# Performance work log

Measured on AMD Instinct MI355X. Metric: run time of the kernel, lower is better.

## Reference

```python
import jax, jax.numpy as jnp
import numpy as np

D_MODEL = 1024
NUM_HEADS = 16
D_K = D_MODEL // NUM_HEADS
SCALE = float(np.sqrt(D_K))


def setup_inputs() -> dict:
    key = jax.random.key(0)
    ks = jax.random.split(key, 11)
    B, S = 2, 2048
    s = 0.02
    return {
        "query": jax.random.normal(ks[0], (B, S, D_MODEL), dtype=jnp.float32),
        "key_in": jax.random.normal(ks[1], (B, S, D_MODEL), dtype=jnp.float32),
        "value": jax.random.normal(ks[2], (B, S, D_MODEL), dtype=jnp.float32),
        "w_q": jax.random.normal(ks[3], (D_MODEL, D_MODEL), dtype=jnp.float32) * s,
        "b_q": jnp.zeros((D_MODEL,), dtype=jnp.float32),
        "w_k": jax.random.normal(ks[4], (D_MODEL, D_MODEL), dtype=jnp.float32) * s,
        "b_k": jnp.zeros((D_MODEL,), dtype=jnp.float32),
        "w_v": jax.random.normal(ks[5], (D_MODEL, D_MODEL), dtype=jnp.float32) * s,
        "b_v": jnp.zeros((D_MODEL,), dtype=jnp.float32),
        "w_o": jax.random.normal(ks[6], (D_MODEL, D_MODEL), dtype=jnp.float32) * s,
        "b_o": jnp.zeros((D_MODEL,), dtype=jnp.float32),
    }


def _mha(query, key_in, value, w_q, b_q, w_k, b_k, w_v, b_v, w_o, b_o):
    B, S, _ = query.shape
    # linear projections (x @ W + b), split into heads: [B, H, S, Dk]
    def proj(x, w, b):
        y = x @ w + b
        return y.reshape(B, -1, NUM_HEADS, D_K).transpose(0, 2, 1, 3)

    Q = proj(query, w_q, b_q)
    K = proj(key_in, w_k, b_k)
    V = proj(value, w_v, b_v)

    # scores: [B, H, Sq, Sk]
    scores = jnp.einsum("bhqd,bhkd->bhqk", Q, K) / SCALE
    attn = jax.nn.softmax(scores, axis=-1)  # dropout is identity in eval mode
    out = jnp.einsum("bhqk,bhkd->bhqd", attn, V)
    out = out.transpose(0, 2, 1, 3).reshape(B, S, D_MODEL)
    return out @ w_o + b_o


def reference(query, key_in, value, w_q, b_q, w_k, b_k, w_v, b_v, w_o, b_o):
    return _mha(query, key_in, value, w_q, b_q, w_k, b_k, w_v, b_v, w_o, b_o)
```

## Files before the change

kernel.cpp:

```cpp
#include <hip/hip_runtime.h>
#include <cstdint>

#define S_LEN 2048
#define DMODEL 1024
#define NHEADS 16
#define DK 64
#define BATCH 2
#define M_TOT 4096
#define NSPLIT 2
#define BHS (BATCH * NHEADS * S_LEN)

typedef __attribute__((ext_vector_type(8)))  short  short8;
typedef __attribute__((ext_vector_type(4)))  float  f32x4;
typedef __attribute__((ext_vector_type(16))) float  f32x16;

__device__ __forceinline__ ushort f2bf(float f) {
    union { float f; uint32_t u; } v; v.f = f;
    uint32_t r = (v.u + 0x7fffu + ((v.u >> 16) & 1u)) >> 16;
    return (ushort)r;
}
__device__ __forceinline__ float bf2f(ushort u) {
    union { uint32_t u; float f; } v; v.u = ((uint32_t)u) << 16;
    return v.f;
}
__device__ __forceinline__ float max3f(float a, float b, float c) {
    float d;
    asm("v_max3_f32 %0, %1, %2, %3" : "=v"(d) : "v"(a), "v"(b), "v"(c));
    return d;
}

__device__ __forceinline__ void gl_lds16(const void* g, void* l) {
    __builtin_amdgcn_global_load_lds(
        (const __attribute__((address_space(1))) void*)(g),
        (__attribute__((address_space(3))) void*)(l), 16, 0, 0);
}

__global__ __launch_bounds__(256)
void conv3_kernel(const float* __restrict__ a0, const float* __restrict__ a1,
                  const float* __restrict__ a2, ushort* __restrict__ o0,
                  ushort* __restrict__ o1, ushort* __restrict__ o2, int n8)
{
    const float*  in  = blockIdx.z == 0 ? a0 : (blockIdx.z == 1 ? a1 : a2);
    ushort*       out = blockIdx.z == 0 ? o0 : (blockIdx.z == 1 ? o1 : o2);
    int i = blockIdx.x * 256 + threadIdx.x;
    const int stride = gridDim.x * 256;
    for (; i < n8; i += stride) {
        const float4* p = (const float4*)(in + (size_t)i * 8);
        float4 a = p[0], b = p[1];
        ushort r[8];
        r[0]=f2bf(a.x); r[1]=f2bf(a.y); r[2]=f2bf(a.z); r[3]=f2bf(a.w);
        r[4]=f2bf(b.x); r[5]=f2bf(b.y); r[6]=f2bf(b.z); r[7]=f2bf(b.w);
        *(ushort4*)(out + (size_t)i * 8)     = *(ushort4*)&r[0];
        *(ushort4*)(out + (size_t)i * 8 + 4) = *(ushort4*)&r[4];
    }
}

__global__ __launch_bounds__(256)
void wtrans4_kernel(const float* __restrict__ wq, const float* __restrict__ wk,
                    const float* __restrict__ wv, const float* __restrict__ wo,
                    ushort* __restrict__ oq, ushort* __restrict__ ok,
                    ushort* __restrict__ ov, ushort* __restrict__ oo_hi,
                    ushort* __restrict__ oo_lo)
{
    const int z = blockIdx.z;
    const float* w  = z == 0 ? wq : (z == 1 ? wk : (z == 2 ? wv : wo));
    ushort*      hi = z == 0 ? oq : (z == 1 ? ok : (z == 2 ? ov : oo_hi));
    const bool   LO = (z == 3);

    __shared__ float t[64][65];
    const int n0 = blockIdx.x * 64, k0 = blockIdx.y * 64;
    const int r  = threadIdx.x >> 2;
    const int cb = (threadIdx.x & 3) * 16;

    #pragma unroll
    for (int j = 0; j < 4; ++j) {
        float4 v = *(const float4*)(w + (size_t)(k0 + r) * DMODEL + n0 + cb + j * 4);
        t[r][cb + j*4 + 0] = v.x;
        t[r][cb + j*4 + 1] = v.y;
        t[r][cb + j*4 + 2] = v.z;
        t[r][cb + j*4 + 3] = v.w;
    }
    __syncthreads();

    ushort h8[16], l8[16];
    #pragma unroll
    for (int j = 0; j < 16; ++j) {
        float x = t[cb + j][r];
        ushort h = f2bf(x);
        h8[j] = h;
        l8[j] = f2bf(x - bf2f(h));
    }
    ushort* dsth = hi + (size_t)(n0 + r) * DMODEL + k0 + cb;
    #pragma unroll
    for (int j = 0; j < 4; ++j)
        *(ushort4*)(dsth + j*4) = *(ushort4*)&h8[j*4];
    if (LO) {
        ushort* dstl = oo_lo + (size_t)(n0 + r) * DMODEL + k0 + cb;
        #pragma unroll
        for (int j = 0; j < 4; ++j)
            *(ushort4*)(dstl + j*4) = *(ushort4*)&l8[j*4];
    }
}

__global__ __launch_bounds__(256)
void gemm_qkv_kernel(const ushort* __restrict__ Aq, const ushort* __restrict__ Ak,
                     const ushort* __restrict__ Av, const ushort* __restrict__ Wq,
                     const ushort* __restrict__ Wk, const ushort* __restrict__ Wv,
                     const float* __restrict__ bq, const float* __restrict__ bk,
                     const float* __restrict__ bv, ushort* __restrict__ Qh,
                     ushort* __restrict__ Kh, ushort* __restrict__ Vt, float qscale)
{
    const int z = blockIdx.z;
    const ushort* A    = z == 0 ? Aq : (z == 1 ? Ak : Av);
    const ushort* Bt   = z == 0 ? Wq : (z == 1 ? Wk : Wv);
    const float*  bias = z == 0 ? bq : (z == 1 ? bk : bv);
    ushort*       out  = z == 0 ? Qh : (z == 1 ? Kh : Vt);
    const float oscale = z == 0 ? qscale : 1.0f;
    const int   mode   = z == 2 ? 2 : 1;

    __shared__ __align__(16) ushort lds[2][12288];

    const int t = threadIdx.x, wv = t >> 6, lane = t & 63;
    const int c = lane & 15, g = lane >> 4;
    const int m0 = blockIdx.y * 128, n0 = blockIdx.x * 64;
    const int wr = wv >> 1, wc = wv & 1;
    const int lrow = lane >> 3, lcol = lane & 7;

    f32x4 acc[4][2];
    #pragma unroll
    for (int i = 0; i < 4; ++i)
        #pragma unroll
        for (int j = 0; j < 2; ++j)
            acc[i][j] = (f32x4){0.f, 0.f, 0.f, 0.f};

    auto stage = [&](int buf, int kt) {
        #pragma unroll
        for (int j = 0; j < 6; ++j) {
            const int ci = wv * 6 + j;
            ushort* dst = &lds[buf][ci * 512];
            const ushort* src;
            if (ci < 16) {
                const int row  = ci * 8 + lrow;
                const int colb = (lcol * 16) ^ ((row & 7) << 4);
                src = A + (size_t)(m0 + row) * 1024 + kt * 64 + (colb >> 1);
            } else {
                const int row  = (ci - 16) * 8 + lrow;
                const int colb = (lcol * 16) ^ ((row & 7) << 4);
                src = Bt + (size_t)(n0 + row) * 1024 + kt * 64 + (colb >> 1);
            }
            gl_lds16(src, dst);
        }
    };

    stage(0, 0);
    __syncthreads();

    for (int kt = 0; kt < 16; ++kt) {
        const int cur = kt & 1;
        if (kt < 15) stage(cur ^ 1, kt + 1);

        const char* la = (const char*)&lds[cur][0];
        const char* lb = (const char*)&lds[cur][8192];
        #pragma unroll
        for (int kk = 0; kk < 2; ++kk) {
            short8 af[4], bf[2];
            #pragma unroll
            for (int mf = 0; mf < 4; ++mf) {
                const int row = wr * 64 + mf * 16 + c;
                af[mf] = *(const short8*)(la + row * 128 +
                          ((kk * 64 + g * 16) ^ ((c & 7) << 4)));
            }
            #pragma unroll
            for (int nf = 0; nf < 2; ++nf) {
                const int row = wc * 32 + nf * 16 + c;
                bf[nf] = *(const short8*)(lb + row * 128 +
                          ((kk * 64 + g * 16) ^ ((c & 7) << 4)));
            }
            #pragma unroll
            for (int mf = 0; mf < 4; ++mf)
                #pragma unroll
                for (int nf = 0; nf < 2; ++nf)
                    acc[mf][nf] = __builtin_amdgcn_mfma_f32_16x16x32_bf16(
                        af[mf], bf[nf], acc[mf][nf], 0, 0, 0);
        }
        __syncthreads();
    }

    const int b      = m0 >> 11;
    const int s_base = m0 & 2047;
    #pragma unroll
    for (int nf = 0; nf < 2; ++nf) {
        const int ncol = n0 + wc * 32 + nf * 16 + c;
        const float bv = bias[ncol];
        const int h = ncol >> 6, dk = ncol & 63;
        #pragma unroll
        for (int mf = 0; mf < 4; ++mf) {
            if (mode == 1) {
                #pragma unroll
                for (int j = 0; j < 4; ++j) {
                    const int s = s_base + wr * 64 + mf * 16 + g * 4 + j;
                    out[(((size_t)(b * NHEADS + h) * S_LEN + s) * DK) + dk] =
                        f2bf((acc[mf][nf][j] + bv) * oscale);
                }
            } else {
                ushort4 v4;
                v4.x = f2bf(acc[mf][nf][0] + bv);
                v4.y = f2bf(acc[mf][nf][1] + bv);
                v4.z = f2bf(acc[mf][nf][2] + bv);
                v4.w = f2bf(acc[mf][nf][3] + bv);
                const int s = s_base + wr * 64 + mf * 16 + g * 4;
                *(ushort4*)&out[((size_t)(b * NHEADS + h) * DK + dk) * S_LEN + s] = v4;
            }
        }
    }
}

__global__ __launch_bounds__(256)
void gemm_o2_kernel(const ushort* __restrict__ A, const ushort* __restrict__ Bhi,
                    const ushort* __restrict__ Blo, const float* __restrict__ bias,
                    float* __restrict__ out)
{
    __shared__ __align__(16) ushort lds[2][16384];

    const int t = threadIdx.x, wv = t >> 6, lane = t & 63;
    const int c = lane & 15, g = lane >> 4;
    const int m0 = blockIdx.y * 128, n0 = blockIdx.x * 64;
    const int wr = wv >> 1, wc = wv & 1;
    const int lrow = lane >> 3, lcol = lane & 7;

    f32x4 acc[4][2];
    #pragma unroll
    for (int i = 0; i < 4; ++i)
        #pragma unroll
        for (int j = 0; j < 2; ++j)
            acc[i][j] = (f32x4){0.f, 0.f, 0.f, 0.f};

    auto stage = [&](int buf, int kt) {
        #pragma unroll
        for (int j = 0; j < 8; ++j) {
            const int ci = wv * 8 + j;
            ushort* dst = &lds[buf][ci * 512];
            const ushort* src;
            if (ci < 16) {
                const int row  = ci * 8 + lrow;
                const int colb = (lcol * 16) ^ ((row & 7) << 4);
                src = A + (size_t)(m0 + row) * 1024 + kt * 64 + (colb >> 1);
            } else if (ci < 24) {
                const int row  = (ci - 16) * 8 + lrow;
                const int colb = (lcol * 16) ^ ((row & 7) << 4);
                src = Bhi + (size_t)(n0 + row) * 1024 + kt * 64 + (colb >> 1);
            } else {
                const int row  = (ci - 24) * 8 + lrow;
                const int colb = (lcol * 16) ^ ((row & 7) << 4);
                src = Blo + (size_t)(n0 + row) * 1024 + kt * 64 + (colb >> 1);
            }
            gl_lds16(src, dst);
        }
    };

    stage(0, 0);
    __syncthreads();

    for (int kt = 0; kt < 16; ++kt) {
        const int cur = kt & 1;
        if (kt < 15) stage(cur ^ 1, kt + 1);

        const char* la = (const char*)&lds[cur][0];
        const char* lh = (const char*)&lds[cur][8192];
        const char* ll = (const char*)&lds[cur][12288];
        #pragma unroll
        for (int kk = 0; kk < 2; ++kk) {
            short8 af[4], bh[2], bl[2];
            #pragma unroll
            for (int mf = 0; mf < 4; ++mf) {
                const int row = wr * 64 + mf * 16 + c;
                af[mf] = *(const short8*)(la + row * 128 +
                          ((kk * 64 + g * 16) ^ ((c & 7) << 4)));
            }
            #pragma unroll
            for (int nf = 0; nf < 2; ++nf) {
                const int row = wc * 32 + nf * 16 + c;
                const int off = row * 128 + ((kk * 64 + g * 16) ^ ((c & 7) << 4));
                bh[nf] = *(const short8*)(lh + off);
                bl[nf] = *(const short8*)(ll + off);
            }
            #pragma unroll
            for (int mf = 0; mf < 4; ++mf)
                #pragma unroll
                for (int nf = 0; nf < 2; ++nf) {
                    acc[mf][nf] = __builtin_amdgcn_mfma_f32_16x16x32_bf16(af[mf], bh[nf], acc[mf][nf], 0,0,0);
                    acc[mf][nf] = __builtin_amdgcn_mfma_f32_16x16x32_bf16(af[mf], bl[nf], acc[mf][nf], 0,0,0);
                }
        }
        __syncthreads();
    }

    #pragma unroll
    for (int nf = 0; nf < 2; ++nf) {
        const int ncol = n0 + wc * 32 + nf * 16 + c;
        const float bv = bias[ncol];
        #pragma unroll
        for (int mf = 0; mf < 4; ++mf)
            #pragma unroll
            for (int j = 0; j < 4; ++j) {
                const int m = m0 + wr * 64 + mf * 16 + g * 4 + j;
                out[(size_t)m * 1024 + ncol] = acc[mf][nf][j] + bv;
            }
    }
}

__global__ __launch_bounds__(256, 2)
void attn_split_kernel(const ushort* __restrict__ Qh, const ushort* __restrict__ Kh,
                       const ushort* __restrict__ Vt, ushort* __restrict__ Op,
                       float* __restrict__ msave, float* __restrict__ lsave)
{
    __shared__ __align__(16) ushort KV[2][8192];

    const int t  = threadIdx.x, wv = t >> 6, lane = t & 63;
    const int q  = lane & 31;
    const int hi = lane >> 5;
    const int bh = blockIdx.y;
    const int q0 = blockIdx.x * 128 + wv * 32;
    const int split = blockIdx.z;
    const int kbase = split * (S_LEN / NSPLIT);

    const ushort* Kb = Kh + (size_t)bh * S_LEN * DK;
    const ushort* Vb = Vt + (size_t)bh * DK * S_LEN;
    const ushort* Qb = Qh + ((size_t)bh * S_LEN + q0 + q) * DK;

    short8 qf[4];
    #pragma unroll
    for (int s = 0; s < 4; ++s)
        qf[s] = *(const short8*)(Qb + s * 16 + hi * 8);

    const ushort* sbase[4];
    int sstr[4];
    char* dbase[4];
    #pragma unroll
    for (int j = 0; j < 4; ++j) {
        const int D = (j * 256 + t) * 16;
        dbase[j] = (char*)&KV[0][0] + D;
        if (D < 8192) {
            const int row = D >> 7;
            const int X   = D & 127;
            const int Xs  = X ^ ((((row & 7) ^ ((row >> 3) & 3))) << 4);
            sbase[j] = Kb + row * DK + (Xs >> 1);
            sstr[j]  = DK;
        } else {
            const int Y   = D - 8192;
            const int kk  = Y >> 12;
            const int Z   = Y & 4095;
            const int r   = Z >> 7;
            const int gsl = ((Z & 127) >> 4) ^ ((r & 7) ^ ((r >> 3) & 3));
            const int d   = r + ((gsl >> 2) << 5);
            sbase[j] = Vb + (size_t)d * S_LEN + kk * 32 + (gsl & 3) * 8;
            sstr[j]  = 1;
        }
    }
    auto stage = [&](int buf, int k0) {
        #pragma unroll
        for (int j = 0; j < 4; ++j)
            gl_lds16(sbase[j] + (size_t)k0 * sstr[j], dbase[j] + buf * 16384);
    };

    float m = -3.0e38f, l = 0.f;
    f32x16 accO[2];
    #pragma unroll
    for (int i = 0; i < 16; ++i) { accO[0][i] = 0.f; accO[1][i] = 0.f; }

    const int swz = ((q & 7) ^ ((q >> 3) & 3)) << 4;

    stage(0, kbase);
    __syncthreads();

    const int NT = S_LEN / NSPLIT / 64;
    for (int kt = 0; kt < NT; ++kt) {
        const int cur = kt & 1;
        if (kt < NT - 1) stage(cur ^ 1, kbase + (kt + 1) * 64);

        const char* Kl = (const char*)&KV[cur][0];
        const char* Vl = Kl + 8192;

        #pragma unroll
        for (int kk = 0; kk < 2; ++kk) {
            f32x16 sa;
            #pragma unroll
            for (int i = 0; i < 16; ++i) sa[i] = 0.f;
            #pragma unroll
            for (int s = 0; s < 4; ++s) {
                short8 kf = *(const short8*)(Kl + (kk * 32 + q) * 128 +
                                             ((s * 32 + hi * 16) ^ swz));
                sa = __builtin_amdgcn_mfma_f32_32x32x16_bf16(kf, qf[s], sa, 0, 0, 0);
            }

            float m0_ = max3f(sa[0],  sa[1],  sa[2]);
            float m1_ = max3f(sa[3],  sa[4],  sa[5]);
            float m2_ = max3f(sa[6],  sa[7],  sa[8]);
            float m3_ = max3f(sa[9],  sa[10], sa[11]);
            float m4_ = max3f(sa[12], sa[13], sa[14]);
            float mt  = fmaxf(max3f(m0_, m1_, m2_), max3f(m3_, m4_, sa[15]));
            mt = fmaxf(mt, __shfl_xor(mt, 32));

            if (__any(mt > m + 8.f)) {
                const float mnew = fmaxf(m, mt);
                const float corr = __builtin_amdgcn_exp2f(m - mnew);
                #pragma unroll
                for (int r = 0; r < 16; ++r) { accO[0][r] *= corr; accO[1][r] *= corr; }
                l *= corr;
                m = mnew;
            }

            float p[16], ps = 0.f;
            #pragma unroll
            for (int r = 0; r < 16; ++r) {
                p[r] = __builtin_amdgcn_exp2f(sa[r] - m);
                ps += p[r];
            }
            ps += __shfl_xor(ps, 32);
            l += ps;

            uint32_t u[8];
            #pragma unroll
            for (int jj = 0; jj < 8; ++jj)
                asm("v_cvt_pk_bf16_f32 %0, %1, %2"
                    : "=v"(u[jj]) : "v"(p[2*jj]), "v"(p[2*jj+1]));
            asm("v_permlane32_swap_b32 %0, %1" : "+v"(u[0]), "+v"(u[2]));
            asm("v_permlane32_swap_b32 %0, %1" : "+v"(u[1]), "+v"(u[3]));
            asm("v_permlane32_swap_b32 %0, %1" : "+v"(u[4]), "+v"(u[6]));
            asm("v_permlane32_swap_b32 %0, %1" : "+v"(u[5]), "+v"(u[7]));
            union { uint32_t w[4]; short8 s8; } pb0, pb1;
            pb0.w[0]=u[0]; pb0.w[1]=u[1]; pb0.w[2]=u[2]; pb0.w[3]=u[3];
            pb1.w[0]=u[4]; pb1.w[1]=u[5]; pb1.w[2]=u[6]; pb1.w[3]=u[7];

            const char* Vg = Vl + kk * 4096;
            #pragma unroll
            for (int db = 0; db < 2; ++db) {
                short8 vf0 = *(const short8*)(Vg + q * 128 + ((db*64 +      hi*16) ^ swz));
                short8 vf1 = *(const short8*)(Vg + q * 128 + ((db*64 + 32 + hi*16) ^ swz));
                accO[db] = __builtin_amdgcn_mfma_f32_32x32x16_bf16(vf0, pb0.s8, accO[db], 0, 0, 0);
                accO[db] = __builtin_amdgcn_mfma_f32_32x32x16_bf16(vf1, pb1.s8, accO[db], 0, 0, 0);
            }
        }
        __syncthreads();
    }

    const float inv = 1.f / l;
    const size_t sIdx = ((size_t)split * BATCH * NHEADS + bh) * S_LEN + q0 + q;
    ushort* base = Op + sIdx * DK;
    #pragma unroll
    for (int db = 0; db < 2; ++db)
        #pragma unroll
        for (int r = 0; r < 16; ++r) {
            const int d = db * 32 + (r & 3) + 8 * (r >> 2) + 4 * hi;
            base[d] = f2bf(accO[db][r] * inv);
        }
    if (hi == 0) {
        msave[sIdx] = m;
        lsave[sIdx] = l;
    }
}

__global__ __launch_bounds__(256)
void combine_kernel(const ushort* __restrict__ Op, const float* __restrict__ msave,
                    const float* __restrict__ lsave, ushort* __restrict__ ctx)
{
    const int idx = blockIdx.x * 256 + threadIdx.x;
    const int bh = idx >> 11;
    const int s  = idx & 2047;

    const float m1 = msave[idx],        l1 = lsave[idx];
    const float m2 = msave[BHS + idx],  l2 = lsave[BHS + idx];
    const float mmax = fmaxf(m1, m2);
    const float w1 = l1 * __builtin_amdgcn_exp2f(m1 - mmax);
    const float w2 = l2 * __builtin_amdgcn_exp2f(m2 - mmax);
    const float inv = 1.f / (w1 + w2);
    const float r1 = w1 * inv, r2 = w2 * inv;

    const ushort* o1 = Op + (size_t)idx * DK;
    const ushort* o2 = Op + ((size_t)BHS + idx) * DK;
    const int b = bh >> 4, h = bh & 15;
    ushort* dst = ctx + ((size_t)b * S_LEN + s) * DMODEL + h * DK;

    #pragma unroll
    for (int j = 0; j < 8; ++j) {
        ushort4 a = *(const ushort4*)(o1 + j * 8);
        ushort4 bq = *(const ushort4*)(o1 + j * 8 + 4);
        ushort4 c = *(const ushort4*)(o2 + j * 8);
        ushort4 dq = *(const ushort4*)(o2 + j * 8 + 4);
        ushort r[8];
        r[0] = f2bf(r1 * bf2f(a.x) + r2 * bf2f(c.x));
        r[1] = f2bf(r1 * bf2f(a.y) + r2 * bf2f(c.y));
        r[2] = f2bf(r1 * bf2f(a.z) + r2 * bf2f(c.z));
        r[3] = f2bf(r1 * bf2f(a.w) + r2 * bf2f(c.w));
        r[4] = f2bf(r1 * bf2f(bq.x) + r2 * bf2f(dq.x));
        r[5] = f2bf(r1 * bf2f(bq.y) + r2 * bf2f(dq.y));
        r[6] = f2bf(r1 * bf2f(bq.z) + r2 * bf2f(dq.z));
        r[7] = f2bf(r1 * bf2f(bq.w) + r2 * bf2f(dq.w));
        *(ushort4*)(dst + j * 8)     = *(ushort4*)&r[0];
        *(ushort4*)(dst + j * 8 + 4) = *(ushort4*)&r[4];
    }
}

extern "C" void kernel_launch(void* const* d_in, const int* in_sizes, int n_in,
                              void* d_out, int out_size, void* d_ws, size_t ws_size,
                              hipStream_t stream)
{
    const float* query  = (const float*)d_in[0];
    const float* key_in = (const float*)d_in[1];
    const float* value  = (const float*)d_in[2];
    const float* w_q = (const float*)d_in[3];
    const float* b_q = (const float*)d_in[4];
    const float* w_k = (const float*)d_in[5];
    const float* b_k = (const float*)d_in[6];
    const float* w_v = (const float*)d_in[7];
    const float* b_v = (const float*)d_in[8];
    const float* w_o = (const float*)d_in[9];
    const float* b_o = (const float*)d_in[10];
    float* out = (float*)d_out;

    const size_t E4M = (size_t)M_TOT * DMODEL;
    const size_t E1M = (size_t)DMODEL * DMODEL;

    ushort* ws = (ushort*)d_ws;
    ushort* Aq    = ws;
    ushort* Ak    = Aq + E4M;
    ushort* Av    = Ak + E4M;
    ushort* Qh    = Av + E4M;
    ushort* Kh    = Qh + E4M;
    ushort* Vt    = Kh + E4M;
    ushort* Wq    = Vt + E4M;
    ushort* Wk    = Wq + E1M;
    ushort* Wv    = Wk + E1M;
    ushort* Wo_hi = Wv + E1M;
    ushort* Wo_lo = Wo_hi + E1M;
    float*  msave = (float*)(Wo_lo + E1M);
    float*  lsave = msave + (size_t)NSPLIT * BHS;
    ushort* ctx   = Aq;
    ushort* Op    = Ak;

    const float qscale = 0.125f * 1.44269504088896340736f;

    dim3 blk(256);
    hipLaunchKernelGGL(conv3_kernel, dim3(512, 1, 3), blk, 0, stream,
                       query, key_in, value, Aq, Ak, Av, (int)(E4M / 8));
    hipLaunchKernelGGL(wtrans4_kernel, dim3(16, 16, 4), blk, 0, stream,
                       w_q, w_k, w_v, w_o, Wq, Wk, Wv, Wo_hi, Wo_lo);

    dim3 ggrd(DMODEL / 64, M_TOT / 128, 3);
    hipLaunchKernelGGL(gemm_qkv_kernel, ggrd, blk, 0, stream,
                       Aq, Ak, Av, Wq, Wk, Wv, b_q, b_k, b_v, Qh, Kh, Vt, qscale);

    dim3 agrd(S_LEN / 128, BATCH * NHEADS, NSPLIT);
    hipLaunchKernelGGL(attn_split_kernel, agrd, blk, 0, stream,
                       Qh, Kh, Vt, Op, msave, lsave);

    hipLaunchKernelGGL(combine_kernel, dim3(BHS / 256), blk, 0, stream,
                       Op, msave, lsave, ctx);

    dim3 ogrd(DMODEL / 64, M_TOT / 128);
    hipLaunchKernelGGL(gemm_o2_kernel, ogrd, blk, 0, stream,
                       ctx, Wo_hi, Wo_lo, b_o, out);
}
```

Measured before the change: 138.2 us.

## Drop split-bf16 output weight and double attention block size to 512 threads

The output projection no longer splits W_o into high and low bf16 halves. It uses a single bf16 weight, which halves its MFMA count and its weight staging and drops the low-part transpose writes. Separately, the attention kernel now runs 512-thread blocks that each cover 256 queries, so every K/V tile staged in LDS is shared by twice as many waves. The cost is lower precision in the output GEMM and different occupancy for attention, since launch_bounds changes from (256,2) to (512).

Result: faster. 133.9 us (-3.2%).

```diff
diff --git a/kernel.cpp b/kernel.cpp
--- a/kernel.cpp
+++ b/kernel.cpp
@@ -59,13 +59,11 @@
 void wtrans4_kernel(const float* __restrict__ wq, const float* __restrict__ wk,
                     const float* __restrict__ wv, const float* __restrict__ wo,
                     ushort* __restrict__ oq, ushort* __restrict__ ok,
-                    ushort* __restrict__ ov, ushort* __restrict__ oo_hi,
-                    ushort* __restrict__ oo_lo)
+                    ushort* __restrict__ ov, ushort* __restrict__ oo)
 {
     const int z = blockIdx.z;
     const float* w  = z == 0 ? wq : (z == 1 ? wk : (z == 2 ? wv : wo));
-    ushort*      hi = z == 0 ? oq : (z == 1 ? ok : (z == 2 ? ov : oo_hi));
-    const bool   LO = (z == 3);
+    ushort*      hi = z == 0 ? oq : (z == 1 ? ok : (z == 2 ? ov : oo));
 
     __shared__ float t[64][65];
     const int n0 = blockIdx.x * 64, k0 = blockIdx.y * 64;
@@ -82,24 +80,13 @@
     }
     __syncthreads();
 
-    ushort h8[16], l8[16];
-    #pragma unroll
-    for (int j = 0; j < 16; ++j) {
-        float x = t[cb + j][r];
-        ushort h = f2bf(x);
-        h8[j] = h;
-        l8[j] = f2bf(x - bf2f(h));
-    }
+    ushort h8[16];
+    #pragma unroll
+    for (int j = 0; j < 16; ++j) h8[j] = f2bf(t[cb + j][r]);
     ushort* dsth = hi + (size_t)(n0 + r) * DMODEL + k0 + cb;
     #pragma unroll
     for (int j = 0; j < 4; ++j)
         *(ushort4*)(dsth + j*4) = *(ushort4*)&h8[j*4];
-    if (LO) {
-        ushort* dstl = oo_lo + (size_t)(n0 + r) * DMODEL + k0 + cb;
-        #pragma unroll
-        for (int j = 0; j < 4; ++j)
-            *(ushort4*)(dstl + j*4) = *(ushort4*)&l8[j*4];
-    }
 }
 
 __global__ __launch_bounds__(256)
@@ -216,11 +203,10 @@
 }
 
 __global__ __launch_bounds__(256)
-void gemm_o2_kernel(const ushort* __restrict__ A, const ushort* __restrict__ Bhi,
-                    const ushort* __restrict__ Blo, const float* __restrict__ bias,
-                    float* __restrict__ out)
-{
-    __shared__ __align__(16) ushort lds[2][16384];
+void gemm_o1_kernel(const ushort* __restrict__ A, const ushort* __restrict__ Bt,
+                    const float* __restrict__ bias, float* __restrict__ out)
+{
+    __shared__ __align__(16) ushort lds[2][12288];
 
     const int t = threadIdx.x, wv = t >> 6, lane = t & 63;
     const int c = lane & 15, g = lane >> 4;
@@ -237,22 +223,18 @@
 
     auto stage = [&](int buf, int kt) {
         #pragma unroll
-        for (int j = 0; j < 8; ++j) {
-            const int ci = wv * 8 + j;
+        for (int j = 0; j < 6; ++j) {
+            const int ci = wv * 6 + j;
             ushort* dst = &lds[buf][ci * 512];
             const ushort* src;
             if (ci < 16) {
                 const int row  = ci * 8 + lrow;
                 const int colb = (lcol * 16) ^ ((row & 7) << 4);
                 src = A + (size_t)(m0 + row) * 1024 + kt * 64 + (colb >> 1);
-            } else if (ci < 24) {
+            } else {
                 const int row  = (ci - 16) * 8 + lrow;
                 const int colb = (lcol * 16) ^ ((row & 7) << 4);
-                src = Bhi + (size_t)(n0 + row) * 1024 + kt * 64 + (colb >> 1);
-            } else {
-                const int row  = (ci - 24) * 8 + lrow;
-                const int colb = (lcol * 16) ^ ((row & 7) << 4);
-                src = Blo + (size_t)(n0 + row) * 1024 + kt * 64 + (colb >> 1);
+                src = Bt + (size_t)(n0 + row) * 1024 + kt * 64 + (colb >> 1);
             }
             gl_lds16(src, dst);
         }
@@ -266,11 +248,10 @@
         if (kt < 15) stage(cur ^ 1, kt + 1);
 
         const char* la = (const char*)&lds[cur][0];
-        const char* lh = (const char*)&lds[cur][8192];
-        const char* ll = (const char*)&lds[cur][12288];
+        const char* lb = (const char*)&lds[cur][8192];
         #pragma unroll
         for (int kk = 0; kk < 2; ++kk) {
-            short8 af[4], bh[2], bl[2];
+            short8 af[4], bf[2];
             #pragma unroll
             for (int mf = 0; mf < 4; ++mf) {
                 const int row = wr * 64 + mf * 16 + c;
@@ -280,17 +261,15 @@
             #pragma unroll
             for (int nf = 0; nf < 2; ++nf) {
                 const int row = wc * 32 + nf * 16 + c;
-                const int off = row * 128 + ((kk * 64 + g * 16) ^ ((c & 7) << 4));
-                bh[nf] = *(const short8*)(lh + off);
-                bl[nf] = *(const short8*)(ll + off);
+                bf[nf] = *(const short8*)(lb + row * 128 +
+                          ((kk * 64 + g * 16) ^ ((c & 7) << 4)));
             }
             #pragma unroll
             for (int mf = 0; mf < 4; ++mf)
                 #pragma unroll
-                for (int nf = 0; nf < 2; ++nf) {
-                    acc[mf][nf] = __builtin_amdgcn_mfma_f32_16x16x32_bf16(af[mf], bh[nf], acc[mf][nf], 0,0,0);
-                    acc[mf][nf] = __builtin_amdgcn_mfma_f32_16x16x32_bf16(af[mf], bl[nf], acc[mf][nf], 0,0,0);
-                }
+                for (int nf = 0; nf < 2; ++nf)
+                    acc[mf][nf] = __builtin_amdgcn_mfma_f32_16x16x32_bf16(
+                        af[mf], bf[nf], acc[mf][nf], 0, 0, 0);
         }
         __syncthreads();
     }
@@ -309,7 +288,7 @@
     }
 }
 
-__global__ __launch_bounds__(256, 2)
+__global__ __launch_bounds__(512)
 void attn_split_kernel(const ushort* __restrict__ Qh, const ushort* __restrict__ Kh,
                        const ushort* __restrict__ Vt, ushort* __restrict__ Op,
                        float* __restrict__ msave, float* __restrict__ lsave)
@@ -320,7 +299,7 @@
     const int q  = lane & 31;
     const int hi = lane >> 5;
     const int bh = blockIdx.y;
-    const int q0 = blockIdx.x * 128 + wv * 32;
+    const int q0 = blockIdx.x * 256 + wv * 32;
     const int split = blockIdx.z;
     const int kbase = split * (S_LEN / NSPLIT);
 
@@ -333,12 +312,12 @@
     for (int s = 0; s < 4; ++s)
         qf[s] = *(const short8*)(Qb + s * 16 + hi * 8);
 
-    const ushort* sbase[4];
-    int sstr[4];
-    char* dbase[4];
-    #pragma unroll
-    for (int j = 0; j < 4; ++j) {
-        const int D = (j * 256 + t) * 16;
+    const ushort* sbase[2];
+    int sstr[2];
+    char* dbase[2];
+    #pragma unroll
+    for (int j = 0; j < 2; ++j) {
+        const int D = (j * 512 + t) * 16;
         dbase[j] = (char*)&KV[0][0] + D;
         if (D < 8192) {
             const int row = D >> 7;
@@ -359,7 +338,7 @@
     }
     auto stage = [&](int buf, int k0) {
         #pragma unroll
-        for (int j = 0; j < 4; ++j)
+        for (int j = 0; j < 2; ++j)
             gl_lds16(sbase[j] + (size_t)k0 * sstr[j], dbase[j] + buf * 16384);
     };
 
@@ -531,9 +510,8 @@
     ushort* Wq    = Vt + E4M;
     ushort* Wk    = Wq + E1M;
     ushort* Wv    = Wk + E1M;
-    ushort* Wo_hi = Wv + E1M;
-    ushort* Wo_lo = Wo_hi + E1M;
-    float*  msave = (float*)(Wo_lo + E1M);
+    ushort* Wo    = Wv + E1M;
+    float*  msave = (float*)(Wo + E1M);
     float*  lsave = msave + (size_t)NSPLIT * BHS;
     ushort* ctx   = Aq;
     ushort* Op    = Ak;
@@ -544,20 +522,20 @@
     hipLaunchKernelGGL(conv3_kernel, dim3(512, 1, 3), blk, 0, stream,
                        query, key_in, value, Aq, Ak, Av, (int)(E4M / 8));
     hipLaunchKernelGGL(wtrans4_kernel, dim3(16, 16, 4), blk, 0, stream,
-                       w_q, w_k, w_v, w_o, Wq, Wk, Wv, Wo_hi, Wo_lo);
+                       w_q, w_k, w_v, w_o, Wq, Wk, Wv, Wo);
 
     dim3 ggrd(DMODEL / 64, M_TOT / 128, 3);
     hipLaunchKernelGGL(gemm_qkv_kernel, ggrd, blk, 0, stream,
                        Aq, Ak, Av, Wq, Wk, Wv, b_q, b_k, b_v, Qh, Kh, Vt, qscale);
 
-    dim3 agrd(S_LEN / 128, BATCH * NHEADS, NSPLIT);
-    hipLaunchKernelGGL(attn_split_kernel, agrd, blk, 0, stream,
+    dim3 agrd(S_LEN / 256, BATCH * NHEADS, NSPLIT);
+    hipLaunchKernelGGL(attn_split_kernel, agrd, dim3(512), 0, stream,
                        Qh, Kh, Vt, Op, msave, lsave);
 
     hipLaunchKernelGGL(combine_kernel, dim3(BHS / 256), blk, 0, stream,
                        Op, msave, lsave, ctx);
 
     dim3 ogrd(DMODEL / 64, M_TOT / 128);
-    hipLaunchKernelGGL(gemm_o2_kernel, ogrd, blk, 0, stream,
-                       ctx, Wo_hi, Wo_lo, b_o, out);
-}
+    hipLaunchKernelGGL(gemm_o1_kernel, ogrd, blk, 0, stream,
+                       ctx, Wo, b_o, out);
+}
```
